# Kernel optimization log

Measured on AMD Instinct MI355X. Metric: run time of the kernel, lower is better.

## Reference

```python
import jax, jax.numpy as jnp
import numpy as np

NEG_INF = -1e9  # Keras uses a large negative for masked logits


def setup_inputs() -> dict:
    key = jax.random.key(0)
    k1, k2, k3, k4, k5 = jax.random.split(key, 5)
    B, Tq, Tv, D, U = 8, 128, 128, 512, 1024
    query = jax.random.normal(k1, (B, Tq, D), dtype=jnp.float32)
    value = jax.random.normal(k2, (B, Tv, D), dtype=jnp.float32)
    mask = jnp.ones((B, Tv), dtype=bool)
    # Dense(units, use_bias=False) kernels and AdditiveAttention scale vector
    W1 = jax.random.normal(k3, (D, U), dtype=jnp.float32) * (1.0 / np.sqrt(D))
    W2 = jax.random.normal(k4, (D, U), dtype=jnp.float32) * (1.0 / np.sqrt(D))
    scale = jax.random.normal(k5, (U,), dtype=jnp.float32) * (1.0 / np.sqrt(U))
    return {"query": query, "value": value, "mask": mask,
            "W1": W1, "W2": W2, "scale": scale}


def reference(query, value, mask, W1, W2, scale):
    # Projections (Dense, no bias)
    wq = jnp.einsum('btd,du->btu', query, W1)   # [B, Tq, U]
    wk = jnp.einsum('bsd,du->bsu', value, W2)   # [B, Tv, U]
    # Additive (Bahdanau) scores: sum_u scale_u * tanh(wq + wk)
    # Materializes [B, Tq, Tv, U] broadcast-add like Keras AdditiveAttention.
    scores = jnp.einsum('u,btsu->bts', scale,
                        jnp.tanh(wq[:, :, None, :] + wk[:, None, :, :]))
    # value mask over key axis (query_mask is all-ones in the source -> no-op)
    scores = jnp.where(mask[:, None, :], scores, NEG_INF)
    attn = jax.nn.softmax(scores, axis=-1)       # [B, Tq, Tv]
    context = jnp.einsum('bts,bsd->btd', attn, value)  # [B, Tq, D]
    return context, attn
```

## Files before the change

kernel.cpp:

```cpp
#include <hip/hip_runtime.h>

#define B_  8
#define TQ  128
#define TV  128
#define DIM 512
#define UU  1024
#define NSPLIT 16
#define NP  (B_ * TQ * TV)
#define C2  2.885390081777927f

typedef __attribute__((ext_vector_type(8))) short     short8;
typedef __attribute__((ext_vector_type(4))) float     f32x4;
typedef __attribute__((ext_vector_type(2))) float     f32x2;
typedef __attribute__((ext_vector_type(4))) unsigned short us4;

__device__ __forceinline__ unsigned short bf16_rtne(float x) {
    unsigned u = __float_as_uint(x);
    unsigned r = u + 0x7FFF + ((u >> 16) & 1);
    return (unsigned short)(r >> 16);
}

__device__ __forceinline__ f32x2 pkfma(f32x2 a, f32x2 b, f32x2 c) {
    return __builtin_elementwise_fma(a, b, c);
}

__global__ __launch_bounds__(256) void k_prep(
    const float* __restrict__ Q, const float* __restrict__ Vv,
    const float* __restrict__ W1, const float* __restrict__ W2,
    unsigned short* __restrict__ Ab, unsigned short* __restrict__ Wh)
{
    __shared__ float ts[32][36];
    const int bx = blockIdx.x;
    const int t  = threadIdx.x;

    if (bx < 1024) {
        int idx = bx * 256 + t;
        int mat = idx >> 17;
        const float* src = mat ? Vv : Q;
        int off = (idx & 131071) * 4;
        float4 v = *(const float4*)&src[off];
        us4 h;
        h.x = bf16_rtne(v.x);
        h.y = bf16_rtne(v.y);
        h.z = bf16_rtne(v.z);
        h.w = bf16_rtne(v.w);
        *(us4*)&Ab[mat * 524288 + off] = h;
    } else {
        int b2   = bx - 1024;
        int mat  = b2 >> 9;
        int tile = b2 & 511;
        int n0 = (tile & 31) * 32;
        int k0 = (tile >> 5) * 32;
        const float* W = mat ? W2 : W1;

        int kk = t >> 3, n4 = (t & 7) * 4;
        float4 w = *(const float4*)&W[(k0 + kk) * UU + n0 + n4];
        ts[n4 + 0][kk] = w.x; ts[n4 + 1][kk] = w.y;
        ts[n4 + 2][kk] = w.z; ts[n4 + 3][kk] = w.w;
        __syncthreads();

        int nn = t >> 3, k4 = (t & 7) * 4;
        float4 v = *(const float4*)&ts[nn][k4];
        us4 h;
        h.x = bf16_rtne(v.x);
        h.y = bf16_rtne(v.y);
        h.z = bf16_rtne(v.z);
        h.w = bf16_rtne(v.w);
        unsigned off = mat * 524288 + (n0 + nn) * 512 + k0 + k4;
        *(us4*)&Wh[off] = h;
    }
}

#define PKP 72
__global__ __launch_bounds__(256) void k_proj(
    const unsigned short* __restrict__ Ab, const unsigned short* __restrict__ Bh,
    float* __restrict__ Eq, float* __restrict__ Ek)
{
    __shared__ short sAb[64 * PKP], sBh[64 * PKP];

    const int tid  = threadIdx.x;
    const int wave = tid >> 6;
    const int lane = tid & 63;

    const int flat = blockIdx.x;
    const int x    = flat & 7;
    const int j    = flat >> 3;
    const int pair = x * 4 + (j >> 4);
    const int nt   = pair & 15;
    const int mat  = pair >> 4;
    const int mt   = j & 15;
    const int m0   = mt * 64;
    const int n0   = nt * 64;

    const unsigned mb = mat * 524288u;
    const int wm = (wave & 1) * 32;
    const int wn = (wave >> 1) * 32;

    const int sm = tid >> 2, sg = tid & 3;
    const unsigned short* gA = Ab + mb + (m0 + sm) * 512;
    const unsigned short* gB = Bh + mb + (n0 + sm) * 512;
    const int so0 = sm * PKP + sg * 8;
    const int so1 = sm * PKP + 32 + sg * 8;

    const int fr = lane & 15, fq = lane >> 4;
    const int aOff0 = (wm + fr) * PKP + fq * 8;
    const int aOff1 = (wm + 16 + fr) * PKP + fq * 8;
    const int bOff0 = (wn + fr) * PKP + fq * 8;
    const int bOff1 = (wn + 16 + fr) * PKP + fq * 8;

    f32x4 acc00 = {0.f, 0.f, 0.f, 0.f};
    f32x4 acc01 = {0.f, 0.f, 0.f, 0.f};
    f32x4 acc10 = {0.f, 0.f, 0.f, 0.f};
    f32x4 acc11 = {0.f, 0.f, 0.f, 0.f};

    int4 rA0, rA1, rB0, rB1;
    #define LOADALL(K)                                                       \
        rA0 = *(const int4*)(gA + (K) + sg * 8);                             \
        rA1 = *(const int4*)(gA + (K) + 32 + sg * 8);                        \
        rB0 = *(const int4*)(gB + (K) + sg * 8);                             \
        rB1 = *(const int4*)(gB + (K) + 32 + sg * 8);

    LOADALL(0)

    #pragma unroll 1
    for (int kc = 0; kc < 8; ++kc) {
        *(int4*)&sAb[so0] = rA0;  *(int4*)&sAb[so1] = rA1;
        *(int4*)&sBh[so0] = rB0;  *(int4*)&sBh[so1] = rB1;
        __syncthreads();

        if (kc < 7) { LOADALL((kc + 1) * 64) }

        #pragma unroll
        for (int ks = 0; ks < 2; ++ks) {
            const int o = ks * 32;
            short8 a0 = *(const short8*)&sAb[aOff0 + o];
            short8 a1 = *(const short8*)&sAb[aOff1 + o];
            short8 b0 = *(const short8*)&sBh[bOff0 + o];
            short8 b1 = *(const short8*)&sBh[bOff1 + o];

            acc00 = __builtin_amdgcn_mfma_f32_16x16x32_bf16(a0, b0, acc00, 0, 0, 0);
            acc01 = __builtin_amdgcn_mfma_f32_16x16x32_bf16(a0, b1, acc01, 0, 0, 0);
            acc10 = __builtin_amdgcn_mfma_f32_16x16x32_bf16(a1, b0, acc10, 0, 0, 0);
            acc11 = __builtin_amdgcn_mfma_f32_16x16x32_bf16(a1, b1, acc11, 0, 0, 0);
        }
        __syncthreads();
    }
    #undef LOADALL

    float* C = mat ? Ek : Eq;
    #pragma unroll
    for (int r = 0; r < 4; ++r) {
        int row0 = m0 + wm + fq * 4 + r;
        int row1 = row0 + 16;
        int col0 = n0 + wn + fr;
        C[row0 * UU + col0]      = __builtin_amdgcn_exp2f(C2 * acc00[r]);
        C[row0 * UU + col0 + 16] = __builtin_amdgcn_exp2f(C2 * acc01[r]);
        C[row1 * UU + col0]      = __builtin_amdgcn_exp2f(C2 * acc10[r]);
        C[row1 * UU + col0 + 16] = __builtin_amdgcn_exp2f(C2 * acc11[r]);
    }
}
#undef PKP

__global__ __launch_bounds__(256) void k_scores(
    const float* __restrict__ Eq, const float* __restrict__ Ek,
    const float* __restrict__ scale, float* __restrict__ part)
{
    __shared__ float qs[64][68];
    __shared__ float ksT[64][68];
    __shared__ float ss[64];

    const int tid = threadIdx.x;
    const int tx  = tid & 15;
    const int ty  = tid >> 4;
    const int b   = blockIdx.z & 7;
    const int us  = blockIdx.z >> 3;
    const int t0  = blockIdx.y * 64;
    const int s0  = blockIdx.x * 64;
    const int u0  = us * (UU / NSPLIT);

    {
        const int r  = tid >> 2;
        const int c0 = (tid & 3) * 16;
        const float* srq = &Eq[(b * TQ + t0 + r) * UU + u0 + c0];
        const float* srk = &Ek[(b * TV + s0 + r) * UU + u0 + c0];
        #pragma unroll
        for (int i = 0; i < 4; ++i) {
            *(float4*)&qs[r][c0 + i * 4] = *(const float4*)(srq + i * 4);
            float4 kv = *(const float4*)(srk + i * 4);
            ksT[c0 + i * 4 + 0][r] = kv.x;
            ksT[c0 + i * 4 + 1][r] = kv.y;
            ksT[c0 + i * 4 + 2][r] = kv.z;
            ksT[c0 + i * 4 + 3][r] = kv.w;
        }
        if (tid < 16)
            *(float4*)&ss[tid * 4] = *(const float4*)&scale[u0 + tid * 4];
    }
    __syncthreads();

    f32x2 acc[4][2] = {};
    const f32x2 one2 = {1.f, 1.f};

    #pragma unroll 2
    for (int u4 = 0; u4 < 16; ++u4) {
        f32x2 kA[4][2];
        #pragma unroll
        for (int uu = 0; uu < 4; ++uu) {
            float4 kv = *(const float4*)&ksT[u4 * 4 + uu][tx * 4];
            kA[uu][0] = (f32x2){kv.x, kv.y};
            kA[uu][1] = (f32x2){kv.z, kv.w};
        }
        const float4 sv = *(const float4*)&ss[u4 * 4];
        const f32x2 sL0 = {sv.x, sv.x}, sH0 = {sv.y, sv.y};
        const f32x2 sL1 = {sv.z, sv.z}, sH1 = {sv.w, sv.w};

        #pragma unroll
        for (int i = 0; i < 4; ++i) {
            const float4 qv = *(const float4*)&qs[ty * 4 + i][u4 * 4];
            const f32x2 qL0 = {qv.x, qv.x}, qH0 = {qv.y, qv.y};
            const f32x2 qL1 = {qv.z, qv.z}, qH1 = {qv.w, qv.w};

            #pragma unroll
            for (int jp = 0; jp < 2; ++jp) {
                f32x2 b1 = pkfma(qL0, kA[0][jp], one2);
                f32x2 b2 = pkfma(qH0, kA[1][jp], one2);
                f32x2 p  = b1 * b2;
                f32x2 n  = pkfma(sH0, b1, sL0 * b2);
                f32x2 r  = {__builtin_amdgcn_rcpf(p.x),
                            __builtin_amdgcn_rcpf(p.y)};
                acc[i][jp] = pkfma(n, r, acc[i][jp]);
                f32x2 b3 = pkfma(qL1, kA[2][jp], one2);
                f32x2 b4 = pkfma(qH1, kA[3][jp], one2);
                f32x2 p2 = b3 * b4;
                f32x2 n2 = pkfma(sH1, b3, sL1 * b4);
                f32x2 r2 = {__builtin_amdgcn_rcpf(p2.x),
                            __builtin_amdgcn_rcpf(p2.y)};
                acc[i][jp] = pkfma(n2, r2, acc[i][jp]);
            }
        }
    }

    #pragma unroll
    for (int i = 0; i < 4; ++i) {
        float4 o = {acc[i][0].x, acc[i][0].y, acc[i][1].x, acc[i][1].y};
        *(float4*)&part[us * NP + (b * TQ + t0 + ty * 4 + i) * TV + s0 + tx * 4] = o;
    }
}

__global__ __launch_bounds__(512) void k_ctx(
    const float* __restrict__ part, const int* __restrict__ mask,
    const float* __restrict__ Vv,
    float* __restrict__ attn, float* __restrict__ ctx)
{
    __shared__ float at[128][20];

    const int tid = threadIdx.x;
    const int dc  = blockIdx.x;
    const int tt  = blockIdx.y;
    const int b   = blockIdx.z;
    const int t0  = tt * 16;

    const int rg = tid >> 5;
    const int ln = tid & 31;
    const int base = (b * TQ + t0 + rg) * TV;

    float4 p4 = {0.f, 0.f, 0.f, 0.f};
    #pragma unroll
    for (int i = 0; i < NSPLIT; ++i) {
        float4 v = *(const float4*)&part[i * NP + base + ln * 4];
        p4.x += v.x; p4.y += v.y; p4.z += v.z; p4.w += v.w;
    }
    const int4 mk = *(const int4*)&mask[b * TV + ln * 4];
    float x[4];
    x[0] = mk.x ? -2.f * p4.x : -1e9f;
    x[1] = mk.y ? -2.f * p4.y : -1e9f;
    x[2] = mk.z ? -2.f * p4.z : -1e9f;
    x[3] = mk.w ? -2.f * p4.w : -1e9f;

    float m = fmaxf(fmaxf(x[0], x[1]), fmaxf(x[2], x[3]));
    #pragma unroll
    for (int o = 16; o > 0; o >>= 1) m = fmaxf(m, __shfl_xor(m, o, 32));
    const float L2E = 1.4426950408889634f;
    float e[4], sum = 0.f;
    #pragma unroll
    for (int j = 0; j < 4; ++j) {
        e[j] = __builtin_amdgcn_exp2f((x[j] - m) * L2E);
        sum += e[j];
    }
    #pragma unroll
    for (int o = 16; o > 0; o >>= 1) sum += __shfl_xor(sum, o, 32);
    const float r = __builtin_amdgcn_rcpf(sum);

    float4 av = {e[0] * r, e[1] * r, e[2] * r, e[3] * r};
    at[ln * 4 + 0][rg] = av.x;
    at[ln * 4 + 1][rg] = av.y;
    at[ln * 4 + 2][rg] = av.z;
    at[ln * 4 + 3][rg] = av.w;
    if (dc == 0) *(float4*)&attn[base + ln * 4] = av;
    __syncthreads();

    const int d  = (tid & 127) + dc * 128;
    const int tg = tid >> 7;
    float acc[4] = {};
    const float* vp = &Vv[b * TV * DIM + d];
    #pragma unroll 4
    for (int s = 0; s < TV; ++s) {
        float v  = vp[s * DIM];
        float4 a = *(const float4*)&at[s][tg * 4];
        acc[0] = fmaf(a.x, v, acc[0]);
        acc[1] = fmaf(a.y, v, acc[1]);
        acc[2] = fmaf(a.z, v, acc[2]);
        acc[3] = fmaf(a.w, v, acc[3]);
    }
    #pragma unroll
    for (int j = 0; j < 4; ++j) {
        int t = t0 + tg * 4 + j;
        ctx[(b * TQ + t) * DIM + d] = acc[j];
    }
}

extern "C" void kernel_launch(void* const* d_in, const int* in_sizes, int n_in,
                              void* d_out, int out_size, void* d_ws, size_t ws_size,
                              hipStream_t stream)
{
    const float* query = (const float*)d_in[0];
    const float* value = (const float*)d_in[1];
    const int*   mask  = (const int*)d_in[2];
    const float* W1    = (const float*)d_in[3];
    const float* W2    = (const float*)d_in[4];
    const float* scale = (const float*)d_in[5];

    float* out  = (float*)d_out;
    float* ctx  = out;
    float* attn = out + B_ * TQ * DIM;

    float* Eq   = (float*)d_ws;
    float* Ek   = Eq + 1024 * 1024;
    float* part = Ek + 1024 * 1024;
    unsigned short* Ab = (unsigned short*)(part + NSPLIT * NP);
    unsigned short* Wh = Ab + 2 * 1024 * 512;

    hipLaunchKernelGGL(k_prep,   dim3(2048),             dim3(256), 0, stream,
                       query, value, W1, W2, Ab, Wh);
    hipLaunchKernelGGL(k_proj,   dim3(512),              dim3(256), 0, stream,
                       Ab, Wh, Eq, Ek);
    hipLaunchKernelGGL(k_scores, dim3(2, 2, 8 * NSPLIT), dim3(256), 0, stream,
                       Eq, Ek, scale, part);
    hipLaunchKernelGGL(k_ctx,    dim3(4, 8, 8),          dim3(512), 0, stream,
                       part, mask, value, attn, ctx);
}
```

Before: 110.7 us.

## Fuse four kernels into one persistent megakernel with grid-wide barriers

```diff
diff --git a/kernel.cpp b/kernel.cpp
--- a/kernel.cpp
+++ b/kernel.cpp
@@ -8,6 +8,7 @@
 #define NSPLIT 16
 #define NP  (B_ * TQ * TV)
 #define C2  2.885390081777927f
+#define NBLK 512u
 
 typedef __attribute__((ext_vector_type(8))) short     short8;
 typedef __attribute__((ext_vector_type(4))) float     f32x4;
@@ -24,299 +25,317 @@
     return __builtin_elementwise_fma(a, b, c);
 }
 
-__global__ __launch_bounds__(256) void k_prep(
+__device__ __forceinline__ void gridbar(unsigned* bar, int idx) {
+    __syncthreads();
+    if (threadIdx.x == 0) {
+        __threadfence();
+        __hip_atomic_fetch_add(&bar[idx], 1u, __ATOMIC_RELEASE,
+                               __HIP_MEMORY_SCOPE_AGENT);
+        while (__hip_atomic_load(&bar[idx], __ATOMIC_RELAXED,
+                                 __HIP_MEMORY_SCOPE_AGENT) < NBLK) {}
+        __threadfence();
+    }
+    __syncthreads();
+}
+
+#define PKP 72
+__global__ __launch_bounds__(256, 2) void k_mega(
     const float* __restrict__ Q, const float* __restrict__ Vv,
+    const int*   __restrict__ mask,
     const float* __restrict__ W1, const float* __restrict__ W2,
-    unsigned short* __restrict__ Ab, unsigned short* __restrict__ Wh)
+    const float* __restrict__ scale,
+    float* __restrict__ attn, float* __restrict__ ctx,
+    float* __restrict__ Eq, float* __restrict__ Ek,
+    float* __restrict__ part,
+    unsigned short* __restrict__ Ab, unsigned short* __restrict__ Wh,
+    unsigned* __restrict__ bar)
 {
-    __shared__ float ts[32][36];
-    const int bx = blockIdx.x;
-    const int t  = threadIdx.x;
-
-    if (bx < 1024) {
-        int idx = bx * 256 + t;
-        int mat = idx >> 17;
-        const float* src = mat ? Vv : Q;
-        int off = (idx & 131071) * 4;
-        float4 v = *(const float4*)&src[off];
-        us4 h;
-        h.x = bf16_rtne(v.x);
-        h.y = bf16_rtne(v.y);
-        h.z = bf16_rtne(v.z);
-        h.w = bf16_rtne(v.w);
-        *(us4*)&Ab[mat * 524288 + off] = h;
+    __shared__ __align__(16) char smem[35072];
+
+    const int tid = threadIdx.x;
+    const int bid = blockIdx.x;
+
+    if (bid < 256) {
+        #pragma unroll
+        for (int it = 0; it < 4; ++it) {
+            int idx = bid * 1024 + it * 256 + tid;
+            int mat = idx >> 17;
+            const float* src = mat ? Vv : Q;
+            int off = (idx & 131071) * 4;
+            float4 v = *(const float4*)&src[off];
+            us4 h;
+            h.x = bf16_rtne(v.x);
+            h.y = bf16_rtne(v.y);
+            h.z = bf16_rtne(v.z);
+            h.w = bf16_rtne(v.w);
+            *(us4*)&Ab[mat * 524288 + off] = h;
+        }
     } else {
-        int b2   = bx - 1024;
-        int mat  = b2 >> 9;
-        int tile = b2 & 511;
-        int n0 = (tile & 31) * 32;
-        int k0 = (tile >> 5) * 32;
-        const float* W = mat ? W2 : W1;
-
-        int kk = t >> 3, n4 = (t & 7) * 4;
-        float4 w = *(const float4*)&W[(k0 + kk) * UU + n0 + n4];
-        ts[n4 + 0][kk] = w.x; ts[n4 + 1][kk] = w.y;
-        ts[n4 + 2][kk] = w.z; ts[n4 + 3][kk] = w.w;
+        float (*ts)[36] = (float(*)[36])smem;
+        #pragma unroll 1
+        for (int it = 0; it < 4; ++it) {
+            int b2   = (bid - 256) * 4 + it;
+            int mat  = b2 >> 9;
+            int tile = b2 & 511;
+            int n0 = (tile & 31) * 32;
+            int k0 = (tile >> 5) * 32;
+            const float* W = mat ? W2 : W1;
+
+            if (it) __syncthreads();
+            int kk = tid >> 3, n4 = (tid & 7) * 4;
+            float4 w = *(const float4*)&W[(k0 + kk) * UU + n0 + n4];
+            ts[n4 + 0][kk] = w.x; ts[n4 + 1][kk] = w.y;
+            ts[n4 + 2][kk] = w.z; ts[n4 + 3][kk] = w.w;
+            __syncthreads();
+
+            int nn = tid >> 3, k4 = (tid & 7) * 4;
+            float4 v = *(const float4*)&ts[nn][k4];
+            us4 h;
+            h.x = bf16_rtne(v.x);
+            h.y = bf16_rtne(v.y);
+            h.z = bf16_rtne(v.z);
+            h.w = bf16_rtne(v.w);
+            unsigned off = mat * 524288 + (n0 + nn) * 512 + k0 + k4;
+            *(us4*)&Wh[off] = h;
+        }
+    }
+    gridbar(bar, 0);
+
+    {
+        short* sAb = (short*)smem;
+        short* sBh = (short*)(smem + 9216);
+
+        const int wave = tid >> 6;
+        const int lane = tid & 63;
+
+        const int x    = bid & 7;
+        const int j    = bid >> 3;
+        const int pair = x * 4 + (j >> 4);
+        const int nt   = pair & 15;
+        const int mat  = pair >> 4;
+        const int mt   = j & 15;
+        const int m0   = mt * 64;
+        const int n0   = nt * 64;
+
+        const unsigned mb = mat * 524288u;
+        const int wm = (wave & 1) * 32;
+        const int wn = (wave >> 1) * 32;
+
+        const int sm = tid >> 2, sg = tid & 3;
+        const unsigned short* gA = Ab + mb + (m0 + sm) * 512;
+        const unsigned short* gB = Wh + mb + (n0 + sm) * 512;
+        const int so0 = sm * PKP + sg * 8;
+        const int so1 = sm * PKP + 32 + sg * 8;
+
+        const int fr = lane & 15, fq = lane >> 4;
+        const int aOff0 = (wm + fr) * PKP + fq * 8;
+        const int aOff1 = (wm + 16 + fr) * PKP + fq * 8;
+        const int bOff0 = (wn + fr) * PKP + fq * 8;
+        const int bOff1 = (wn + 16 + fr) * PKP + fq * 8;
+
+        f32x4 acc00 = {0.f, 0.f, 0.f, 0.f};
+        f32x4 acc01 = {0.f, 0.f, 0.f, 0.f};
+        f32x4 acc10 = {0.f, 0.f, 0.f, 0.f};
+        f32x4 acc11 = {0.f, 0.f, 0.f, 0.f};
+
+        int4 rA0, rA1, rB0, rB1;
+        #define LOADALL(K)                                                   \
+            rA0 = *(const int4*)(gA + (K) + sg * 8);                         \
+            rA1 = *(const int4*)(gA + (K) + 32 + sg * 8);                    \
+            rB0 = *(const int4*)(gB + (K) + sg * 8);                         \
+            rB1 = *(const int4*)(gB + (K) + 32 + sg * 8);
+
+        LOADALL(0)
+
+        #pragma unroll 1
+        for (int kc = 0; kc < 8; ++kc) {
+            *(int4*)&sAb[so0] = rA0;  *(int4*)&sAb[so1] = rA1;
+            *(int4*)&sBh[so0] = rB0;  *(int4*)&sBh[so1] = rB1;
+            __syncthreads();
+
+            if (kc < 7) { LOADALL((kc + 1) * 64) }
+
+            #pragma unroll
+            for (int ks = 0; ks < 2; ++ks) {
+                const int o = ks * 32;
+                short8 a0 = *(const short8*)&sAb[aOff0 + o];
+                short8 a1 = *(const short8*)&sAb[aOff1 + o];
+                short8 b0 = *(const short8*)&sBh[bOff0 + o];
+                short8 b1 = *(const short8*)&sBh[bOff1 + o];
+
+                acc00 = __builtin_amdgcn_mfma_f32_16x16x32_bf16(a0, b0, acc00, 0, 0, 0);
+                acc01 = __builtin_amdgcn_mfma_f32_16x16x32_bf16(a0, b1, acc01, 0, 0, 0);
+                acc10 = __builtin_amdgcn_mfma_f32_16x16x32_bf16(a1, b0, acc10, 0, 0, 0);
+                acc11 = __builtin_amdgcn_mfma_f32_16x16x32_bf16(a1, b1, acc11, 0, 0, 0);
+            }
+            __syncthreads();
+        }
+        #undef LOADALL
+
+        float* C = mat ? Ek : Eq;
+        #pragma unroll
+        for (int r = 0; r < 4; ++r) {
+            int row0 = m0 + wm + fq * 4 + r;
+            int row1 = row0 + 16;
+            int col0 = n0 + wn + fr;
+            C[row0 * UU + col0]      = __builtin_amdgcn_exp2f(C2 * acc00[r]);
+            C[row0 * UU + col0 + 16] = __builtin_amdgcn_exp2f(C2 * acc01[r]);
+            C[row1 * UU + col0]      = __builtin_amdgcn_exp2f(C2 * acc10[r]);
+            C[row1 * UU + col0 + 16] = __builtin_amdgcn_exp2f(C2 * acc11[r]);
+        }
+    }
+    gridbar(bar, 1);
+
+    {
+        float (*qs)[68]  = (float(*)[68])smem;
+        float (*ksT)[68] = (float(*)[68])(smem + 17408);
+        float* ss        = (float*)(smem + 34816);
+
+        const int tx  = tid & 15;
+        const int ty  = tid >> 4;
+        const int bz  = bid >> 2;
+        const int b   = bz & 7;
+        const int us  = bz >> 3;
+        const int t0  = ((bid >> 1) & 1) * 64;
+        const int s0  = (bid & 1) * 64;
+        const int u0  = us * (UU / NSPLIT);
+
+        {
+            const int r  = tid >> 2;
+            const int c0 = (tid & 3) * 16;
+            const float* srq = &Eq[(b * TQ + t0 + r) * UU + u0 + c0];
+            const float* srk = &Ek[(b * TV + s0 + r) * UU + u0 + c0];
+            #pragma unroll
+            for (int i = 0; i < 4; ++i) {
+                *(float4*)&qs[r][c0 + i * 4] = *(const float4*)(srq + i * 4);
+                float4 kv = *(const float4*)(srk + i * 4);
+                ksT[c0 + i * 4 + 0][r] = kv.x;
+                ksT[c0 + i * 4 + 1][r] = kv.y;
+                ksT[c0 + i * 4 + 2][r] = kv.z;
+                ksT[c0 + i * 4 + 3][r] = kv.w;
+            }
+            if (tid < 16)
+                *(float4*)&ss[tid * 4] = *(const float4*)&scale[u0 + tid * 4];
+        }
         __syncthreads();
 
-        int nn = t >> 3, k4 = (t & 7) * 4;
-        float4 v = *(const float4*)&ts[nn][k4];
-        us4 h;
-        h.x = bf16_rtne(v.x);
-        h.y = bf16_rtne(v.y);
-        h.z = bf16_rtne(v.z);
-        h.w = bf16_rtne(v.w);
-        unsigned off = mat * 524288 + (n0 + nn) * 512 + k0 + k4;
-        *(us4*)&Wh[off] = h;
-    }
-}
-
-#define PKP 72
-__global__ __launch_bounds__(256) void k_proj(
-    const unsigned short* __restrict__ Ab, const unsigned short* __restrict__ Bh,
-    float* __restrict__ Eq, float* __restrict__ Ek)
-{
-    __shared__ short sAb[64 * PKP], sBh[64 * PKP];
-
-    const int tid  = threadIdx.x;
-    const int wave = tid >> 6;
-    const int lane = tid & 63;
-
-    const int flat = blockIdx.x;
-    const int x    = flat & 7;
-    const int j    = flat >> 3;
-    const int pair = x * 4 + (j >> 4);
-    const int nt   = pair & 15;
-    const int mat  = pair >> 4;
-    const int mt   = j & 15;
-    const int m0   = mt * 64;
-    const int n0   = nt * 64;
-
-    const unsigned mb = mat * 524288u;
-    const int wm = (wave & 1) * 32;
-    const int wn = (wave >> 1) * 32;
-
-    const int sm = tid >> 2, sg = tid & 3;
-    const unsigned short* gA = Ab + mb + (m0 + sm) * 512;
-    const unsigned short* gB = Bh + mb + (n0 + sm) * 512;
-    const int so0 = sm * PKP + sg * 8;
-    const int so1 = sm * PKP + 32 + sg * 8;
-
-    const int fr = lane & 15, fq = lane >> 4;
-    const int aOff0 = (wm + fr) * PKP + fq * 8;
-    const int aOff1 = (wm + 16 + fr) * PKP + fq * 8;
-    const int bOff0 = (wn + fr) * PKP + fq * 8;
-    const int bOff1 = (wn + 16 + fr) * PKP + fq * 8;
-
-    f32x4 acc00 = {0.f, 0.f, 0.f, 0.f};
-    f32x4 acc01 = {0.f, 0.f, 0.f, 0.f};
-    f32x4 acc10 = {0.f, 0.f, 0.f, 0.f};
-    f32x4 acc11 = {0.f, 0.f, 0.f, 0.f};
-
-    int4 rA0, rA1, rB0, rB1;
-    #define LOADALL(K)                                                       \
-        rA0 = *(const int4*)(gA + (K) + sg * 8);                             \
-        rA1 = *(const int4*)(gA + (K) + 32 + sg * 8);                        \
-        rB0 = *(const int4*)(gB + (K) + sg * 8);                             \
-        rB1 = *(const int4*)(gB + (K) + 32 + sg * 8);
-
-    LOADALL(0)
-
-    #pragma unroll 1
-    for (int kc = 0; kc < 8; ++kc) {
-        *(int4*)&sAb[so0] = rA0;  *(int4*)&sAb[so1] = rA1;
-        *(int4*)&sBh[so0] = rB0;  *(int4*)&sBh[so1] = rB1;
+        f32x2 acc[4][2] = {};
+        const f32x2 one2 = {1.f, 1.f};
+
+        #pragma unroll 2
+        for (int u4 = 0; u4 < 16; ++u4) {
+            f32x2 kA[4][2];
+            #pragma unroll
+            for (int uu = 0; uu < 4; ++uu) {
+                float4 kv = *(const float4*)&ksT[u4 * 4 + uu][tx * 4];
+                kA[uu][0] = (f32x2){kv.x, kv.y};
+                kA[uu][1] = (f32x2){kv.z, kv.w};
+            }
+            const float4 sv = *(const float4*)&ss[u4 * 4];
+            const f32x2 sL0 = {sv.x, sv.x}, sH0 = {sv.y, sv.y};
+            const f32x2 sL1 = {sv.z, sv.z}, sH1 = {sv.w, sv.w};
+
+            #pragma unroll
+            for (int i = 0; i < 4; ++i) {
+                const float4 qv = *(const float4*)&qs[ty * 4 + i][u4 * 4];
+                const f32x2 qL0 = {qv.x, qv.x}, qH0 = {qv.y, qv.y};
+                const f32x2 qL1 = {qv.z, qv.z}, qH1 = {qv.w, qv.w};
+
+                #pragma unroll
+                for (int jp = 0; jp < 2; ++jp) {
+                    f32x2 b1 = pkfma(qL0, kA[0][jp], one2);
+                    f32x2 b2 = pkfma(qH0, kA[1][jp], one2);
+                    f32x2 p  = b1 * b2;
+                    f32x2 n  = pkfma(sH0, b1, sL0 * b2);
+                    f32x2 r  = {__builtin_amdgcn_rcpf(p.x),
+                                __builtin_amdgcn_rcpf(p.y)};
+                    acc[i][jp] = pkfma(n, r, acc[i][jp]);
+                    f32x2 b3 = pkfma(qL1, kA[2][jp], one2);
+                    f32x2 b4 = pkfma(qH1, kA[3][jp], one2);
+                    f32x2 p2 = b3 * b4;
+                    f32x2 n2 = pkfma(sH1, b3, sL1 * b4);
+                    f32x2 r2 = {__builtin_amdgcn_rcpf(p2.x),
+                                __builtin_amdgcn_rcpf(p2.y)};
+                    acc[i][jp] = pkfma(n2, r2, acc[i][jp]);
+                }
+            }
+        }
+
+        #pragma unroll
+        for (int i = 0; i < 4; ++i) {
+            float4 o = {acc[i][0].x, acc[i][0].y, acc[i][1].x, acc[i][1].y};
+            *(float4*)&part[us * NP + (b * TQ + t0 + ty * 4 + i) * TV + s0 + tx * 4] = o;
+        }
+    }
+    gridbar(bar, 2);
+
+    {
+        float (*at)[12] = (float(*)[12])smem;
+
+        const int dc = bid & 3;
+        const int tt = (bid >> 2) & 15;
+        const int b  = bid >> 6;
+        const int t0 = tt * 8;
+        const int rg = tid >> 5;
+        const int ln = tid & 31;
+        const int base = (b * TQ + t0 + rg) * TV;
+
+        float4 p4 = {0.f, 0.f, 0.f, 0.f};
+        #pragma unroll
+        for (int i = 0; i < NSPLIT; ++i) {
+            float4 v = *(const float4*)&part[i * NP + base + ln * 4];
+            p4.x += v.x; p4.y += v.y; p4.z += v.z; p4.w += v.w;
+        }
+        const int4 mk = *(const int4*)&mask[b * TV + ln * 4];
+        float x[4];
+        x[0] = mk.x ? -2.f * p4.x : -1e9f;
+        x[1] = mk.y ? -2.f * p4.y : -1e9f;
+        x[2] = mk.z ? -2.f * p4.z : -1e9f;
+        x[3] = mk.w ? -2.f * p4.w : -1e9f;
+
+        float m = fmaxf(fmaxf(x[0], x[1]), fmaxf(x[2], x[3]));
+        #pragma unroll
+        for (int o = 16; o > 0; o >>= 1) m = fmaxf(m, __shfl_xor(m, o, 32));
+        const float L2E = 1.4426950408889634f;
+        float e[4], sum = 0.f;
+        #pragma unroll
+        for (int jj = 0; jj < 4; ++jj) {
+            e[jj] = __builtin_amdgcn_exp2f((x[jj] - m) * L2E);
+            sum += e[jj];
+        }
+        #pragma unroll
+        for (int o = 16; o > 0; o >>= 1) sum += __shfl_xor(sum, o, 32);
+        const float r = __builtin_amdgcn_rcpf(sum);
+
+        float4 av = {e[0] * r, e[1] * r, e[2] * r, e[3] * r};
+        at[ln * 4 + 0][rg] = av.x;
+        at[ln * 4 + 1][rg] = av.y;
+        at[ln * 4 + 2][rg] = av.z;
+        at[ln * 4 + 3][rg] = av.w;
+        if (dc == 0) *(float4*)&attn[base + ln * 4] = av;
         __syncthreads();
 
-        if (kc < 7) { LOADALL((kc + 1) * 64) }
-
-        #pragma unroll
-        for (int ks = 0; ks < 2; ++ks) {
-            const int o = ks * 32;
-            short8 a0 = *(const short8*)&sAb[aOff0 + o];
-            short8 a1 = *(const short8*)&sAb[aOff1 + o];
-            short8 b0 = *(const short8*)&sBh[bOff0 + o];
-            short8 b1 = *(const short8*)&sBh[bOff1 + o];
-
-            acc00 = __builtin_amdgcn_mfma_f32_16x16x32_bf16(a0, b0, acc00, 0, 0, 0);
-            acc01 = __builtin_amdgcn_mfma_f32_16x16x32_bf16(a0, b1, acc01, 0, 0, 0);
-            acc10 = __builtin_amdgcn_mfma_f32_16x16x32_bf16(a1, b0, acc10, 0, 0, 0);
-            acc11 = __builtin_amdgcn_mfma_f32_16x16x32_bf16(a1, b1, acc11, 0, 0, 0);
-        }
-        __syncthreads();
-    }
-    #undef LOADALL
-
-    float* C = mat ? Ek : Eq;
-    #pragma unroll
-    for (int r = 0; r < 4; ++r) {
-        int row0 = m0 + wm + fq * 4 + r;
-        int row1 = row0 + 16;
-        int col0 = n0 + wn + fr;
-        C[row0 * UU + col0]      = __builtin_amdgcn_exp2f(C2 * acc00[r]);
-        C[row0 * UU + col0 + 16] = __builtin_amdgcn_exp2f(C2 * acc01[r]);
-        C[row1 * UU + col0]      = __builtin_amdgcn_exp2f(C2 * acc10[r]);
-        C[row1 * UU + col0 + 16] = __builtin_amdgcn_exp2f(C2 * acc11[r]);
+        const int d  = (tid & 127) + dc * 128;
+        const int tg = tid >> 7;
+        float acc[4] = {};
+        const float* vp = &Vv[b * TV * DIM + d];
+        #pragma unroll 4
+        for (int s = 0; s < TV; ++s) {
+            float v  = vp[s * DIM];
+            float4 a = *(const float4*)&at[s][tg * 4];
+            acc[0] = fmaf(a.x, v, acc[0]);
+            acc[1] = fmaf(a.y, v, acc[1]);
+            acc[2] = fmaf(a.z, v, acc[2]);
+            acc[3] = fmaf(a.w, v, acc[3]);
+        }
+        #pragma unroll
+        for (int jj = 0; jj < 4; ++jj) {
+            int t = t0 + tg * 4 + jj;
+            ctx[(b * TQ + t) * DIM + d] = acc[jj];
+        }
     }
 }
 #undef PKP
-
-__global__ __launch_bounds__(256) void k_scores(
-    const float* __restrict__ Eq, const float* __restrict__ Ek,
-    const float* __restrict__ scale, float* __restrict__ part)
-{
-    __shared__ float qs[64][68];
-    __shared__ float ksT[64][68];
-    __shared__ float ss[64];
-
-    const int tid = threadIdx.x;
-    const int tx  = tid & 15;
-    const int ty  = tid >> 4;
-    const int b   = blockIdx.z & 7;
-    const int us  = blockIdx.z >> 3;
-    const int t0  = blockIdx.y * 64;
-    const int s0  = blockIdx.x * 64;
-    const int u0  = us * (UU / NSPLIT);
-
-    {
-        const int r  = tid >> 2;
-        const int c0 = (tid & 3) * 16;
-        const float* srq = &Eq[(b * TQ + t0 + r) * UU + u0 + c0];
-        const float* srk = &Ek[(b * TV + s0 + r) * UU + u0 + c0];
-        #pragma unroll
-        for (int i = 0; i < 4; ++i) {
-            *(float4*)&qs[r][c0 + i * 4] = *(const float4*)(srq + i * 4);
-            float4 kv = *(const float4*)(srk + i * 4);
-            ksT[c0 + i * 4 + 0][r] = kv.x;
-            ksT[c0 + i * 4 + 1][r] = kv.y;
-            ksT[c0 + i * 4 + 2][r] = kv.z;
-            ksT[c0 + i * 4 + 3][r] = kv.w;
-        }
-        if (tid < 16)
-            *(float4*)&ss[tid * 4] = *(const float4*)&scale[u0 + tid * 4];
-    }
-    __syncthreads();
-
-    f32x2 acc[4][2] = {};
-    const f32x2 one2 = {1.f, 1.f};
-
-    #pragma unroll 2
-    for (int u4 = 0; u4 < 16; ++u4) {
-        f32x2 kA[4][2];
-        #pragma unroll
-        for (int uu = 0; uu < 4; ++uu) {
-            float4 kv = *(const float4*)&ksT[u4 * 4 + uu][tx * 4];
-            kA[uu][0] = (f32x2){kv.x, kv.y};
-            kA[uu][1] = (f32x2){kv.z, kv.w};
-        }
-        const float4 sv = *(const float4*)&ss[u4 * 4];
-        const f32x2 sL0 = {sv.x, sv.x}, sH0 = {sv.y, sv.y};
-        const f32x2 sL1 = {sv.z, sv.z}, sH1 = {sv.w, sv.w};
-
-        #pragma unroll
-        for (int i = 0; i < 4; ++i) {
-            const float4 qv = *(const float4*)&qs[ty * 4 + i][u4 * 4];
-            const f32x2 qL0 = {qv.x, qv.x}, qH0 = {qv.y, qv.y};
-            const f32x2 qL1 = {qv.z, qv.z}, qH1 = {qv.w, qv.w};
-
-            #pragma unroll
-            for (int jp = 0; jp < 2; ++jp) {
-                f32x2 b1 = pkfma(qL0, kA[0][jp], one2);
-                f32x2 b2 = pkfma(qH0, kA[1][jp], one2);
-                f32x2 p  = b1 * b2;
-                f32x2 n  = pkfma(sH0, b1, sL0 * b2);
-                f32x2 r  = {__builtin_amdgcn_rcpf(p.x),
-                            __builtin_amdgcn_rcpf(p.y)};
-                acc[i][jp] = pkfma(n, r, acc[i][jp]);
-                f32x2 b3 = pkfma(qL1, kA[2][jp], one2);
-                f32x2 b4 = pkfma(qH1, kA[3][jp], one2);
-                f32x2 p2 = b3 * b4;
-                f32x2 n2 = pkfma(sH1, b3, sL1 * b4);
-                f32x2 r2 = {__builtin_amdgcn_rcpf(p2.x),
-                            __builtin_amdgcn_rcpf(p2.y)};
-                acc[i][jp] = pkfma(n2, r2, acc[i][jp]);
-            }
-        }
-    }
-
-    #pragma unroll
-    for (int i = 0; i < 4; ++i) {
-        float4 o = {acc[i][0].x, acc[i][0].y, acc[i][1].x, acc[i][1].y};
-        *(float4*)&part[us * NP + (b * TQ + t0 + ty * 4 + i) * TV + s0 + tx * 4] = o;
-    }
-}
-
-__global__ __launch_bounds__(512) void k_ctx(
-    const float* __restrict__ part, const int* __restrict__ mask,
-    const float* __restrict__ Vv,
-    float* __restrict__ attn, float* __restrict__ ctx)
-{
-    __shared__ float at[128][20];
-
-    const int tid = threadIdx.x;
-    const int dc  = blockIdx.x;
-    const int tt  = blockIdx.y;
-    const int b   = blockIdx.z;
-    const int t0  = tt * 16;
-
-    const int rg = tid >> 5;
-    const int ln = tid & 31;
-    const int base = (b * TQ + t0 + rg) * TV;
-
-    float4 p4 = {0.f, 0.f, 0.f, 0.f};
-    #pragma unroll
-    for (int i = 0; i < NSPLIT; ++i) {
-        float4 v = *(const float4*)&part[i * NP + base + ln * 4];
-        p4.x += v.x; p4.y += v.y; p4.z += v.z; p4.w += v.w;
-    }
-    const int4 mk = *(const int4*)&mask[b * TV + ln * 4];
-    float x[4];
-    x[0] = mk.x ? -2.f * p4.x : -1e9f;
-    x[1] = mk.y ? -2.f * p4.y : -1e9f;
-    x[2] = mk.z ? -2.f * p4.z : -1e9f;
-    x[3] = mk.w ? -2.f * p4.w : -1e9f;
-
-    float m = fmaxf(fmaxf(x[0], x[1]), fmaxf(x[2], x[3]));
-    #pragma unroll
-    for (int o = 16; o > 0; o >>= 1) m = fmaxf(m, __shfl_xor(m, o, 32));
-    const float L2E = 1.4426950408889634f;
-    float e[4], sum = 0.f;
-    #pragma unroll
-    for (int j = 0; j < 4; ++j) {
-        e[j] = __builtin_amdgcn_exp2f((x[j] - m) * L2E);
-        sum += e[j];
-    }
-    #pragma unroll
-    for (int o = 16; o > 0; o >>= 1) sum += __shfl_xor(sum, o, 32);
-    const float r = __builtin_amdgcn_rcpf(sum);
-
-    float4 av = {e[0] * r, e[1] * r, e[2] * r, e[3] * r};
-    at[ln * 4 + 0][rg] = av.x;
-    at[ln * 4 + 1][rg] = av.y;
-    at[ln * 4 + 2][rg] = av.z;
-    at[ln * 4 + 3][rg] = av.w;
-    if (dc == 0) *(float4*)&attn[base + ln * 4] = av;
-    __syncthreads();
-
-    const int d  = (tid & 127) + dc * 128;
-    const int tg = tid >> 7;
-    float acc[4] = {};
-    const float* vp = &Vv[b * TV * DIM + d];
-    #pragma unroll 4
-    for (int s = 0; s < TV; ++s) {
-        float v  = vp[s * DIM];
-        float4 a = *(const float4*)&at[s][tg * 4];
-        acc[0] = fmaf(a.x, v, acc[0]);
-        acc[1] = fmaf(a.y, v, acc[1]);
-        acc[2] = fmaf(a.z, v, acc[2]);
-        acc[3] = fmaf(a.w, v, acc[3]);
-    }
-    #pragma unroll
-    for (int j = 0; j < 4; ++j) {
-        int t = t0 + tg * 4 + j;
-        ctx[(b * TQ + t) * DIM + d] = acc[j];
-    }
-}
 
 extern "C" void kernel_launch(void* const* d_in, const int* in_sizes, int n_in,
                               void* d_out, int out_size, void* d_ws, size_t ws_size,
@@ -338,13 +357,10 @@
     float* part = Ek + 1024 * 1024;
     unsigned short* Ab = (unsigned short*)(part + NSPLIT * NP);
     unsigned short* Wh = Ab + 2 * 1024 * 512;
-
-    hipLaunchKernelGGL(k_prep,   dim3(2048),             dim3(256), 0, stream,
-                       query, value, W1, W2, Ab, Wh);
-    hipLaunchKernelGGL(k_proj,   dim3(512),              dim3(256), 0, stream,
-                       Ab, Wh, Eq, Ek);
-    hipLaunchKernelGGL(k_scores, dim3(2, 2, 8 * NSPLIT), dim3(256), 0, stream,
-                       Eq, Ek, scale, part);
-    hipLaunchKernelGGL(k_ctx,    dim3(4, 8, 8),          dim3(512), 0, stream,
-                       part, mask, value, attn, ctx);
-}
+    unsigned* bar = (unsigned*)(Wh + 2 * 1024 * 512);
+
+    hipMemsetAsync(bar, 0, 16, stream);
+    hipLaunchKernelGGL(k_mega, dim3(512), dim3(256), 0, stream,
+                       query, value, mask, W1, W2, scale, attn, ctx,
+                       Eq, Ek, part, Ab, Wh, bar);
+}
```

Measured after the change: 275.1 us. +148.4%, slower.
